# Optimization experiments

Hardware: AMD Instinct MI355X
Metric: run time of the kernel (lower is better)

Reference implementation:

```python
import jax, jax.numpy as jnp
import numpy as np

B, C, D, J = 8, 2048, 128, 128

def setup_inputs() -> dict:
    key = jax.random.key(0)
    ks = jax.random.split(key, 24)
    s = 0.02
    inp = {
        "operation_features": jax.random.normal(ks[0], (B, C, D), jnp.float32),
        "relations": jax.random.randint(ks[1], (B, C - 2, 2), 0, C, jnp.int64),
        "begins_idx": jax.random.randint(ks[2], (B, J), 0, C, jnp.int64),
        "ends_idx": jax.random.randint(ks[3], (B, J), 0, C, jnp.int64),
        "same_type_mask": (jax.random.uniform(ks[4], (B, C, C)) > 0.5).astype(jnp.float32),
        # BeginEndEncoder
        "W_begin": jax.random.normal(ks[5], (D, D), jnp.float32) * s,
        "b_begin": jnp.zeros((D,), jnp.float32),
        "W_end": jax.random.normal(ks[6], (D, D), jnp.float32) * s,
        "b_end": jnp.zeros((D,), jnp.float32),
        # OperationTimeRelationEncoder.mix: Linear(3D -> D)
        "W_mix3": jax.random.normal(ks[7], (3 * D, D), jnp.float32) * s,
        "b_mix3": jnp.zeros((D,), jnp.float32),
        # SelfAttention (hidden_dim = D)
        "W_qkv": jax.random.normal(ks[8], (D, 3 * D), jnp.float32) * s,
        "b_qkv": jnp.zeros((3 * D,), jnp.float32),
        "w_score": jax.random.normal(ks[9], (2 * D,), jnp.float32) * s,
        "b_score": jnp.zeros((), jnp.float32),
        "W_out": jax.random.normal(ks[10], (D, D), jnp.float32) * s,
        "b_out": jnp.zeros((D,), jnp.float32),
        # block mix: Linear(2D -> D)
        "W_mix2": jax.random.normal(ks[11], (2 * D, D), jnp.float32) * s,
        "b_mix2": jnp.zeros((D,), jnp.float32),
    }
    return inp

def _gather_ops(ops, idx):
    # ops: [B,C,D], idx: [B,M] -> [B,M,D]  (torch.gather along dim 1 with expanded index)
    Bb, _, Dd = ops.shape
    M = idx.shape[1]
    return jnp.take_along_axis(ops, jnp.broadcast_to(idx[:, :, None], (Bb, M, Dd)), axis=1)

def reference(operation_features, relations, begins_idx, ends_idx, same_type_mask,
              W_begin, b_begin, W_end, b_end, W_mix3, b_mix3,
              W_qkv, b_qkv, w_score, b_score, W_out, b_out, W_mix2, b_mix2):
    ops = operation_features
    Dd = ops.shape[-1]
    # --- OperationTimeRelationEncoder ---
    pred = _gather_ops(ops, relations[..., 0])      # [B,C-2,D]
    succ = _gather_ops(ops, relations[..., 1])      # [B,C-2,D]
    concated = jnp.concatenate([ops[:, :-2, :], pred, succ], axis=-1)  # [B,C-2,3D]
    mixed = concated @ W_mix3 + b_mix3              # [B,C-2,D]
    begin_f = _gather_ops(ops, begins_idx) @ W_begin + b_begin  # [B,J,D]
    end_f = _gather_ops(ops, ends_idx) @ W_end + b_end
    begin = jnp.mean(begin_f, axis=1)               # [B,D]
    end = jnp.mean(end_f, axis=1)
    seq = jnp.concatenate([mixed, begin[:, None, :], end[:, None, :]], axis=1)  # [B,C,D]
    # --- SelfAttention (GAT-style additive score, decomposed to avoid CxCx2h blowup) ---
    qkv = ops @ W_qkv + b_qkv                       # [B,C,3D]
    q, k, v = jnp.split(qkv, 3, axis=-1)
    sq = q @ w_score[:Dd]                           # [B,C]  q_i . w_q
    sk = k @ w_score[Dd:]                           # [B,C]  k_j . w_k
    scores = jax.nn.leaky_relu(sq[:, :, None] + sk[:, None, :] + b_score)  # [B,C,C]
    attn = jax.nn.softmax(scores * same_type_mask, axis=-1)                # multiplicative mask, as in torch
    weighted = jnp.einsum('bij,bjd->bid', attn, v)  # [B,C,D]
    same_type = weighted @ W_out + b_out            # [B,C,D]
    # --- final mix ---
    return jnp.concatenate([seq, same_type], axis=-1) @ W_mix2 + b_mix2  # [B,C,D]
```

## Files before the change

### kernel.cpp

```cpp
#include <hip/hip_runtime.h>
#include <cstddef>

typedef __bf16 bf16;
typedef __bf16 bf16x4 __attribute__((ext_vector_type(4)));
typedef __bf16 bf16x8 __attribute__((ext_vector_type(8)));
typedef float  f32x4  __attribute__((ext_vector_type(4)));

#define MFMA16(a, b, c) __builtin_amdgcn_mfma_f32_16x16x32_bf16((a), (b), (c), 0, 0, 0)

#define BB 8
#define CC 2048
#define DD 128
#define JJN 128

#define WS_PK    ((size_t)0)
#define WS_OATT  ((size_t)4194304)
#define WS_OPS16 ((size_t)8388608)
#define WS_SQF   ((size_t)12582912)
#define WS_SKF   ((size_t)12648448)
#define WS_G1T   ((size_t)12713984)
#define WS_G2T   ((size_t)12746752)
#define WS_G3T   ((size_t)12779520)
#define WS_WCT   ((size_t)12812288)
#define WS_GBT   ((size_t)12845056)
#define WS_GET   ((size_t)12877824)
#define WS_UQK   ((size_t)12910592)
#define WS_BBM   ((size_t)12911104)
#define WS_BBB   ((size_t)12911616)
#define WS_BBE   ((size_t)12912128)
#define WS_SC    ((size_t)12912640)
#define WS_WCN   ((size_t)12913152)
#define WS_GBN   ((size_t)12945920)
#define WS_GEN   ((size_t)12978688)

__global__ __launch_bounds__(256) void k_prepcast(
    const float* __restrict__ ops, bf16* __restrict__ ops16,
    const float* __restrict__ Wmix3, const float* __restrict__ Wmix2,
    const float* __restrict__ Wout,  const float* __restrict__ Wbegin,
    const float* __restrict__ Wend,  const float* __restrict__ Wqkv,
    const float* __restrict__ bqkv,  const float* __restrict__ wscore,
    const float* __restrict__ bscore,const float* __restrict__ bmix3,
    const float* __restrict__ bout,  const float* __restrict__ bmix2,
    const float* __restrict__ bbegin,const float* __restrict__ bend,
    bf16* __restrict__ G1T, bf16* __restrict__ G2T, bf16* __restrict__ G3T,
    bf16* __restrict__ WCT, bf16* __restrict__ GBT, bf16* __restrict__ GET,
    bf16* __restrict__ WCN, bf16* __restrict__ GBN, bf16* __restrict__ GEN,
    bf16* __restrict__ uqk, float* __restrict__ BBM, float* __restrict__ BBB,
    float* __restrict__ BBE, float* __restrict__ sc)
{
    __shared__ bf16  LshT[128 * 132];
    __shared__ float Rsh[128 * 8];
    int wg = blockIdx.x;
    int t  = threadIdx.x;

    if (wg == 0) {
        for (int half = 0; half < 2; ++half) {
            #pragma unroll
            for (int pass = 0; pass < 16; ++pass) {
                int idx = pass * 256 + t;
                int d   = idx >> 5;
                int e0  = (idx & 31) * 4;
                f32x4 v = *(const f32x4*)(Wqkv + d*384 + half*128 + e0);
                #pragma unroll
                for (int jj = 0; jj < 4; ++jj)
                    LshT[(e0 + jj)*132 + d] = (bf16)v[jj];
            }
            if (t < 32) {
                f32x4 wv = *(const f32x4*)(wscore + half*128 + t*4);
                #pragma unroll
                for (int jj = 0; jj < 4; ++jj) Rsh[t*4 + jj] = wv[jj];
            }
            __syncthreads();
            if (t < 128) {
                float s = 0.f;
                for (int e = 0; e < 128; ++e)
                    s += (float)LshT[e*132 + t] * Rsh[e];
                uqk[half*128 + t] = (bf16)s;
            }
            __syncthreads();
        }
        float bm = 0.f, bb_ = 0.f, be_ = 0.f, bon = 0.f;
        for (int half = 0; half < 2; ++half) {
            #pragma unroll
            for (int pass = 0; pass < 16; ++pass) {
                int idx = pass * 256 + t;
                int f   = idx >> 5;
                int e0  = (idx & 31) * 4;
                f32x4 v = *(const f32x4*)(Wmix2 + (size_t)(half*128 + f)*128 + e0);
                #pragma unroll
                for (int jj = 0; jj < 4; ++jj)
                    LshT[f*132 + e0 + jj] = (bf16)v[jj];
            }
            if (t < 32) {
                if (half == 0) {
                    f32x4 v0 = *(const f32x4*)(bmix3  + t*4);
                    f32x4 v1 = *(const f32x4*)(bbegin + t*4);
                    f32x4 v2 = *(const f32x4*)(bend   + t*4);
                    #pragma unroll
                    for (int jj = 0; jj < 4; ++jj) {
                        Rsh[t*4 + jj]       = v0[jj];
                        Rsh[128 + t*4 + jj] = v1[jj];
                        Rsh[256 + t*4 + jj] = v2[jj];
                    }
                } else {
                    f32x4 v3 = *(const f32x4*)(bout + t*4);
                    #pragma unroll
                    for (int jj = 0; jj < 4; ++jj) Rsh[t*4 + jj] = v3[jj];
                }
            }
            __syncthreads();
            if (t < 128) {
                if (half == 0) {
                    for (int f = 0; f < 128; ++f) {
                        float wv = (float)LshT[f*132 + t];
                        bm  += Rsh[f]       * wv;
                        bb_ += Rsh[128 + f] * wv;
                        be_ += Rsh[256 + f] * wv;
                    }
                } else {
                    for (int f = 0; f < 128; ++f)
                        bon += Rsh[f] * (float)LshT[f*132 + t];
                }
            }
            __syncthreads();
        }
        if (t < 128) {
            float bm2 = bmix2[t];
            BBM[t] = bm  + bon + bm2;
            BBB[t] = bb_ + bon + bm2;
            BBE[t] = be_ + bon + bm2;
        }
        if (t >= 128) {
            int e2 = t - 128;
            Rsh[512 + e2] = bqkv[e2]       * wscore[e2];
            Rsh[640 + e2] = bqkv[128 + e2] * wscore[128 + e2];
        }
        __syncthreads();
        if (t == 0) {
            float cq = 0.f, ck = 0.f;
            for (int e2 = 0; e2 < 128; ++e2) {
                cq += Rsh[512 + e2];
                ck += Rsh[640 + e2];
            }
            sc[0] = cq + bscore[0];
            sc[1] = ck;
        }
        return;
    }
    if (wg <= 96) {
        int id  = wg - 1;
        int mat = id >> 4, sub = id & 15;
        const float* L; const float* R; bf16* O; bf16* O2;
        switch (mat) {
            case 0: L = Wmix3;           R = Wmix2;           O = G1T; O2 = nullptr; break;
            case 1: L = Wmix3 + 128*128; R = Wmix2;           O = G2T; O2 = nullptr; break;
            case 2: L = Wmix3 + 256*128; R = Wmix2;           O = G3T; O2 = nullptr; break;
            case 3: L = Wout;            R = Wmix2 + 128*128; O = WCT; O2 = WCN; break;
            case 4: L = Wbegin;          R = Wmix2;           O = GBT; O2 = GBN; break;
            default:L = Wend;            R = Wmix2;           O = GET; O2 = GEN; break;
        }
        int e0 = sub * 8;
        #pragma unroll
        for (int pass = 0; pass < 16; ++pass) {
            int idx = pass * 256 + t;
            int d   = idx >> 5;
            int f0  = (idx & 31) * 4;
            f32x4 v = *(const f32x4*)(L + d * 128 + f0);
            #pragma unroll
            for (int jj = 0; jj < 4; ++jj)
                LshT[(f0 + jj) * 132 + d] = (bf16)v[jj];
        }
        #pragma unroll
        for (int pass = 0; pass < 4; ++pass) {
            int idx = pass * 256 + t;
            int f   = idx >> 3;
            int ee  = idx & 7;
            Rsh[f * 8 + ee] = R[f * 128 + e0 + ee];
        }
        __syncthreads();
        int ee = t >> 5;
        int e  = e0 + ee;
        int d0 = (t & 31) * 4;
        float s[4] = {0.f, 0.f, 0.f, 0.f};
        for (int f = 0; f < 128; ++f) {
            bf16x4 lv = *(const bf16x4*)&LshT[f * 132 + d0];
            float rv = Rsh[f * 8 + ee];
            #pragma unroll
            for (int dd = 0; dd < 4; ++dd)
                s[dd] += (float)lv[dd] * rv;
        }
        #pragma unroll
        for (int dd = 0; dd < 4; ++dd) {
            O[e * 128 + d0 + dd] = (bf16)s[dd];
            if (O2) O2[(d0 + dd) * 128 + e] = (bf16)s[dd];
        }
        return;
    }
    size_t i = (size_t)(wg - 97) * 256 + t;
    f32x4 a = *(const f32x4*)(ops + i * 8);
    f32x4 b = *(const f32x4*)(ops + i * 8 + 4);
    bf16x8 o;
    #pragma unroll
    for (int e = 0; e < 4; ++e) { o[e] = (bf16)a[e]; o[4 + e] = (bf16)b[e]; }
    *(bf16x8*)(ops16 + i * 8) = o;
}

__global__ __launch_bounds__(256) void k_v(
    const bf16* __restrict__ ops16, const float* __restrict__ Wqkv,
    const float* __restrict__ bqkv, const bf16* __restrict__ uqk,
    const float* __restrict__ sc,
    bf16* __restrict__ PK, float* __restrict__ sqf, float* __restrict__ skf)
{
    __shared__ bf16 A[144 * 136];
    int b  = blockIdx.x >> 4;
    int jt = (blockIdx.x & 15) * 128;
    int t  = threadIdx.x;
    #pragma unroll
    for (int pass = 0; pass < 16; ++pass) {
        int idx = pass * 256 + t;
        int d   = idx >> 5;
        int n0  = (idx & 31) * 4;
        f32x4 v = *(const f32x4*)(Wqkv + d*384 + 256 + n0);
        #pragma unroll
        for (int jj = 0; jj < 4; ++jj)
            A[(n0 + jj)*136 + d] = (bf16)v[jj];
    }
    {
        int row = t >> 7, col = t & 127;
        A[(128 + row)*136 + col] = uqk[row*128 + col];
    }
    for (int idx = t; idx < 14*136; idx += 256)
        A[130*136 + idx] = (bf16)0.f;
    __syncthreads();

    int lane = t & 63, w = t >> 6;
    int m = lane & 15, q = lane >> 4;
    f32x4 acc[9][2];
    #pragma unroll
    for (int rb = 0; rb < 9; ++rb)
        #pragma unroll
        for (int cb = 0; cb < 2; ++cb)
            acc[rb][cb] = {0.f, 0.f, 0.f, 0.f};

    const bf16* opsb = ops16 + (size_t)b * CC * DD;
    #pragma unroll
    for (int kc = 0; kc < 4; ++kc) {
        bf16x8 bfr[2];
        #pragma unroll
        for (int cb = 0; cb < 2; ++cb) {
            int j = jt + w*32 + cb*16 + m;
            bfr[cb] = *(const bf16x8*)(opsb + (size_t)j*DD + kc*32 + q*8);
        }
        #pragma unroll
        for (int rb = 0; rb < 9; ++rb) {
            bf16x8 afr = *(const bf16x8*)&A[(rb*16 + m)*136 + kc*32 + q*8];
            acc[rb][0] = MFMA16(afr, bfr[0], acc[rb][0]);
            acc[rb][1] = MFMA16(afr, bfr[1], acc[rb][1]);
        }
    }
    float cqb = sc[0], ckv = sc[1];
    #pragma unroll
    for (int cb = 0; cb < 2; ++cb) {
        int j = jt + w*32 + cb*16 + m;
        if (q == 0) {
            sqf[b*CC + j] = acc[8][cb][0] + cqb;
            skf[b*CC + j] = acc[8][cb][1] + ckv;
        }
    }
    __syncthreads();
    bf16* pack = A;
    #pragma unroll
    for (int cb = 0; cb < 2; ++cb) {
        int qq_base = cb*2 + (m>>3);
        int e       = m & 7;
        #pragma unroll
        for (int rb = 0; rb < 8; ++rb) {
            #pragma unroll
            for (int r = 0; r < 4; ++r) {
                float v = acc[rb][cb][r] + bqkv[256 + rb*16 + q*4 + r];
                pack[w*4096 + rb*512 + qq_base*128 + (q*4+r)*8 + e] = (bf16)v;
            }
        }
    }
    __syncthreads();
    bf16* pkb = PK + (size_t)b * DD * CC + (size_t)jt * 128;
    #pragma unroll
    for (int pass = 0; pass < 8; ++pass) {
        int lidx = pass * 256 + t;
        *(uint4*)(pkb + (size_t)lidx * 8) = *(const uint4*)&pack[lidx * 8];
    }
}

struct MaskLd { f32x4 v[8]; };

__device__ __forceinline__ MaskLd stage_load(const float* __restrict__ mrow0,
                                             int st, int lane)
{
    MaskLd L;
    int rr0 = lane >> 4, cc = (lane & 15) * 4;
    const float* src = mrow0 + st * 64 + cc;
    #pragma unroll
    for (int k = 0; k < 8; ++k)
        L.v[k] = __builtin_nontemporal_load(
            (const f32x4*)(src + ((size_t)(rr0 + k * 4)) * CC));
    return L;
}

__device__ __forceinline__ void stage_write(const MaskLd& L, bf16* mb,
                                            int buf, int lane)
{
    int rr0 = lane >> 4, cc = (lane & 15) * 4;
    bf16* dst = mb + buf * 2816;
    #pragma unroll
    for (int k = 0; k < 8; ++k) {
        bf16x4 o;
        #pragma unroll
        for (int e = 0; e < 4; ++e) o[e] = (bf16)L.v[k][e];
        *(bf16x4*)(dst + (rr0 + k * 4) * 88 + cc) = o;
    }
}

__device__ __forceinline__ void load_vb(const bf16* __restrict__ pkb, int jc,
                                        int q, int m, bf16x8 vb[8])
{
    #pragma unroll
    for (int nb = 0; nb < 8; ++nb)
        vb[nb] = *(const bf16x8*)(pkb + ((size_t)(((jc*8 + nb)*4 + q)*16 + m)) * 8);
}

__device__ __forceinline__ void substep(const bf16* mb, const float* skb,
    int buf, int st, int sub, int tile, int q, int m, float sq,
    const bf16x8 vb[8], float& lsum, f32x4 acc[8])
{
    bf16x8 mk = *(const bf16x8*)(mb + buf * 2816 + (tile*16 + m) * 88
                                 + sub * 32 + q * 8);
    int jo = st * 64 + sub * 32 + q * 8;
    f32x4 s0 = *(const f32x4*)(skb + jo);
    f32x4 s1 = *(const f32x4*)(skb + jo + 4);
    float sks[8] = {s0[0], s0[1], s0[2], s0[3], s1[0], s1[1], s1[2], s1[3]};
    bf16x8 a;
    #pragma unroll
    for (int e = 0; e < 8; ++e) {
        float tv = sq + sks[e];
        float lr = fmaxf(tv, 0.01f * tv);
        float z  = lr * (float)mk[e];
        float p  = __expf(z);
        lsum += p;
        a[e] = (bf16)p;
    }
    #pragma unroll
    for (int nb = 0; nb < 8; ++nb)
        acc[nb] = MFMA16(a, vb[nb], acc[nb]);
}

__global__ __launch_bounds__(256) void k_att(
    const float* __restrict__ mask, const bf16* __restrict__ PK,
    const float* __restrict__ sqf, const float* __restrict__ skf,
    bf16* __restrict__ Oatt)
{
    __shared__ __align__(16) char smem[53248];
    int t    = threadIdx.x;
    int lane = t & 63, w = t >> 6;
    int b    = blockIdx.x & 7;
    int i0   = (blockIdx.x >> 3) << 5;
    int m = lane & 15, q = lane >> 4;

    bf16*  mbuf = (bf16*)(smem + w * 11264);
    float* skb  = (float*)(smem + 45056 + w * 2048);

    {
        const float* src = skf + b*CC + w*512;
        f32x4 v0 = *(const f32x4*)(src + lane*4);
        f32x4 v1 = *(const f32x4*)(src + 256 + lane*4);
        *(f32x4*)(skb + lane*4) = v0;
        *(f32x4*)(skb + 256 + lane*4) = v1;
    }
    float sq0 = sqf[b*CC + i0 + m];
    float sq1 = sqf[b*CC + i0 + 16 + m];
    const float* mrow0 = mask + ((size_t)(b*CC + i0))*CC + w*512;
    const bf16*  pkb   = PK + (size_t)b * DD * CC;
    int jc0 = w * 16;

    f32x4 acc0[8], acc1[8];
    #pragma unroll
    for (int nb = 0; nb < 8; ++nb) {
        acc0[nb] = {0.f, 0.f, 0.f, 0.f};
        acc1[nb] = {0.f, 0.f, 0.f, 0.f};
    }
    float lsum0 = 0.f, lsum1 = 0.f;

    {   MaskLd r0 = stage_load(mrow0, 0, lane);
        stage_write(r0, mbuf, 0, lane); }
    MaskLd r1 = stage_load(mrow0, 1, lane);
    MaskLd r2 = stage_load(mrow0, 2, lane);

    int buf = 0;
    for (int st = 0; st < 8; ++st) {
        #pragma unroll
        for (int sub = 0; sub < 2; ++sub) {
            bf16x8 vb[8];
            load_vb(pkb, jc0 + st*2 + sub, q, m, vb);
            substep(mbuf, skb, buf, st, sub, 0, q, m, sq0, vb, lsum0, acc0);
            substep(mbuf, skb, buf, st, sub, 1, q, m, sq1, vb, lsum1, acc1);
        }
        if (st + 1 < 8) stage_write(r1, mbuf, buf ^ 1, lane);
        r1 = r2;
        if (st + 3 < 8) r2 = stage_load(mrow0, st + 3, lane);
        buf ^= 1;
    }

    __syncthreads();
    float* Osh = (float*)smem;
    float* Lsh = (float*)(smem + 33792);
    #pragma unroll
    for (int tile = 0; tile < 2; ++tile) {
        float ls = tile ? lsum1 : lsum0;
        ls += __shfl_xor(ls, 16, 64);
        ls += __shfl_xor(ls, 32, 64);
        if (q == 0) Lsh[w*16 + m] = ls;
        const f32x4* acc = tile ? acc1 : acc0;
        #pragma unroll
        for (int nb = 0; nb < 8; ++nb)
            #pragma unroll
            for (int r = 0; r < 4; ++r)
                Osh[(w*16 + q*4 + r)*132 + nb*16 + m] = acc[nb][r];
        __syncthreads();

        int r  = t >> 4;
        int c0 = (t & 15) * 8;
        float l = Lsh[r] + Lsh[16 + r] + Lsh[32 + r] + Lsh[48 + r];
        float inv = 1.0f / l;
        bf16x8 o;
        #pragma unroll
        for (int e = 0; e < 8; ++e) {
            float s = Osh[r*132 + c0 + e] + Osh[(16 + r)*132 + c0 + e]
                    + Osh[(32 + r)*132 + c0 + e] + Osh[(48 + r)*132 + c0 + e];
            o[e] = (bf16)(s * inv);
        }
        *(bf16x8*)(Oatt + ((size_t)(b*CC) + i0 + tile*16 + r)*DD + c0) = o;
        if (tile == 0) __syncthreads();
    }
}

__global__ __launch_bounds__(256) void k_epi(
    const bf16* __restrict__ ops16, const int* __restrict__ relations,
    const int* __restrict__ begins, const int* __restrict__ ends,
    const bf16* __restrict__ Oatt,
    const bf16* __restrict__ G1T, const bf16* __restrict__ G2T,
    const bf16* __restrict__ G3T, const bf16* __restrict__ WCT,
    const bf16* __restrict__ GBN, const bf16* __restrict__ GEN,
    const bf16* __restrict__ WCN,
    const float* __restrict__ BBM, const float* __restrict__ BBB,
    const float* __restrict__ BBE, float* __restrict__ out)
{
    __shared__ bf16 Abuf[32 * 136];
    __shared__ bf16 Bbuf[128 * 136];
    int t  = threadIdx.x;

    if (blockIdx.x < 8) {
        __shared__ float meanv[2][128];
        int eidx  = blockIdx.x * 2 + (t >> 7);
        int b     = eidx >> 1, which = eidx & 1;
        int tl    = t & 127;
        const int* idx = which ? (ends + b*JJN) : (begins + b*JJN);
        const bf16* opsb = ops16 + (size_t)b * CC * DD;
        float s0 = 0.f, s1 = 0.f;
        for (int j = 0; j < JJN; j += 2) {
            int r0 = idx[j], r1 = idx[j+1];
            s0 += (float)opsb[(size_t)r0*DD + tl];
            s1 += (float)opsb[(size_t)r1*DD + tl];
        }
        meanv[t >> 7][tl] = (s0 + s1) * (1.0f / (float)JJN);
        __syncthreads();
        const bf16* G   = which ? GEN : GBN;
        const float* Bv = which ? BBE : BBB;
        const bf16* orow = Oatt + ((size_t)b*CC + (CC - 2 + which)) * DD;
        float a = Bv[tl];
        const float* mv = meanv[t >> 7];
        for (int d = 0; d < 128; ++d) {
            a += mv[d] * (float)G[d*128 + tl];
            a += (float)orow[d] * (float)WCN[d*128 + tl];
        }
        out[((size_t)b*CC + (CC - 2 + which))*DD + tl] = a;
        return;
    }

    int gid = blockIdx.x - 8;
    int b  = gid >> 6;
    int c0 = (gid & 63) * 32;
    int lane = t & 63, w = t >> 6;
    int m = lane & 15, q = lane >> 4;

    f32x4 acc[2][2];
    #pragma unroll
    for (int rb = 0; rb < 2; ++rb)
        #pragma unroll
        for (int cb = 0; cb < 2; ++cb)
            acc[rb][cb] = {0.f, 0.f, 0.f, 0.f};

    const bf16* Bsrc[4] = {G1T, G2T, G3T, WCT};
    int arow = t >> 3, ao = (t & 7) * 16;
    int brow = t >> 1, bo = (t & 1) * 64;
    int c = c0 + arow;

    for (int term = 0; term < 4; ++term) {
        const bf16* src;
        if (term == 0)      src = ops16 + ((size_t)(b*CC + c)) * DD;
        else if (term == 3) src = Oatt  + ((size_t)(b*CC + c)) * DD;
        else {
            int ridx = relations[((size_t)b*(CC-2) + min(c, CC-3))*2 + (term - 1)];
            src = ops16 + ((size_t)(b*CC) + ridx) * DD;
        }
        *(uint4*)&Abuf[arow*136 + ao]     = *(const uint4*)(src + ao);
        *(uint4*)&Abuf[arow*136 + ao + 8] = *(const uint4*)(src + ao + 8);

        const uint4* bs = (const uint4*)(Bsrc[term] + brow*128 + bo);
        uint4* bd = (uint4*)&Bbuf[brow*136 + bo];
        #pragma unroll
        for (int ii = 0; ii < 8; ++ii) bd[ii] = bs[ii];
        __syncthreads();

        #pragma unroll
        for (int kc = 0; kc < 4; ++kc) {
            bf16x8 bfr[2];
            #pragma unroll
            for (int cb = 0; cb < 2; ++cb)
                bfr[cb] = *(const bf16x8*)&Bbuf[(w*32 + cb*16 + m)*136 + kc*32 + q*8];
            #pragma unroll
            for (int rb = 0; rb < 2; ++rb) {
                bf16x8 afr = *(const bf16x8*)&Abuf[(rb*16 + m)*136 + kc*32 + q*8];
                acc[rb][0] = MFMA16(afr, bfr[0], acc[rb][0]);
                acc[rb][1] = MFMA16(afr, bfr[1], acc[rb][1]);
            }
        }
        __syncthreads();
    }
    #pragma unroll
    for (int cb = 0; cb < 2; ++cb) {
        int col = w*32 + cb*16 + m;
        float bias = BBM[col];
        #pragma unroll
        for (int rb = 0; rb < 2; ++rb) {
            #pragma unroll
            for (int r = 0; r < 4; ++r) {
                int cg = c0 + rb*16 + q*4 + r;
                if (cg < CC - 2)
                    out[((size_t)(b*CC) + cg)*DD + col] = acc[rb][cb][r] + bias;
            }
        }
    }
}

extern "C" void kernel_launch(void* const* d_in, const int* in_sizes, int n_in,
                              void* d_out, int out_size, void* d_ws, size_t ws_size,
                              hipStream_t stream)
{
    const float* ops      = (const float*)d_in[0];
    const int*  relations = (const int*)d_in[1];
    const int*  begins    = (const int*)d_in[2];
    const int*  ends      = (const int*)d_in[3];
    const float* mask     = (const float*)d_in[4];
    const float* Wbegin   = (const float*)d_in[5];
    const float* bbegin   = (const float*)d_in[6];
    const float* Wend     = (const float*)d_in[7];
    const float* bend     = (const float*)d_in[8];
    const float* Wmix3    = (const float*)d_in[9];
    const float* bmix3    = (const float*)d_in[10];
    const float* Wqkv     = (const float*)d_in[11];
    const float* bqkv     = (const float*)d_in[12];
    const float* wscore   = (const float*)d_in[13];
    const float* bscore   = (const float*)d_in[14];
    const float* Wout     = (const float*)d_in[15];
    const float* bout     = (const float*)d_in[16];
    const float* Wmix2    = (const float*)d_in[17];
    const float* bmix2    = (const float*)d_in[18];
    float* outp = (float*)d_out;

    char* ws = (char*)d_ws;
    bf16*  PK    = (bf16*)(ws + WS_PK);
    bf16*  Oatt  = (bf16*)(ws + WS_OATT);
    bf16*  OPS16 = (bf16*)(ws + WS_OPS16);
    float* sqf   = (float*)(ws + WS_SQF);
    float* skf   = (float*)(ws + WS_SKF);
    bf16*  G1T   = (bf16*)(ws + WS_G1T);
    bf16*  G2T   = (bf16*)(ws + WS_G2T);
    bf16*  G3T   = (bf16*)(ws + WS_G3T);
    bf16*  WCT   = (bf16*)(ws + WS_WCT);
    bf16*  GBT   = (bf16*)(ws + WS_GBT);
    bf16*  GET   = (bf16*)(ws + WS_GET);
    bf16*  WCN   = (bf16*)(ws + WS_WCN);
    bf16*  GBN   = (bf16*)(ws + WS_GBN);
    bf16*  GEN   = (bf16*)(ws + WS_GEN);
    bf16*  UQK   = (bf16*)(ws + WS_UQK);
    float* BBM   = (float*)(ws + WS_BBM);
    float* BBB   = (float*)(ws + WS_BBB);
    float* BBE   = (float*)(ws + WS_BBE);
    float* SC    = (float*)(ws + WS_SC);

    k_prepcast<<<dim3(1121), dim3(256), 0, stream>>>(
        ops, OPS16,
        Wmix3, Wmix2, Wout, Wbegin, Wend, Wqkv, bqkv, wscore, bscore,
        bmix3, bout, bmix2, bbegin, bend,
        G1T, G2T, G3T, WCT, GBT, GET, WCN, GBN, GEN,
        UQK, BBM, BBB, BBE, SC);

    k_v<<<dim3(128), dim3(256), 0, stream>>>(
        OPS16, Wqkv, bqkv, UQK, SC, PK, sqf, skf);

    k_att<<<dim3(512), dim3(256), 0, stream>>>(
        mask, PK, sqf, skf, Oatt);

    k_epi<<<dim3(520), dim3(256), 0, stream>>>(
        OPS16, relations, begins, ends, Oatt,
        G1T, G2T, G3T, WCT, GBN, GEN, WCN, BBM, BBB, BBE, outp);
}
```

Baseline: 283.4 us.

## Pre-pack mask to bits and fuse attention with epilogue GEMM

The float mask is converted to a packed bitmask in the prep kernel, and the attention loop reads mask bytes from LDS instead of staging float tiles. The attention and epilogue kernels are merged so the normalized attention output stays in shared memory rather than round-tripping through global memory. The begin/end means are also moved into the prep kernel. Binarizing assumes the mask holds only zeros and ones, and the full mask read now happens before attention instead of overlapping with it.

Result: faster. 275.2 us (median of 2 runs) (-2.9%).

```diff
diff --git a/kernel.cpp b/kernel.cpp
--- a/kernel.cpp
+++ b/kernel.cpp
@@ -32,9 +32,13 @@
 #define WS_WCN   ((size_t)12913152)
 #define WS_GBN   ((size_t)12945920)
 #define WS_GEN   ((size_t)12978688)
+#define WS_MB    ((size_t)13011456)
+#define WS_MEANV ((size_t)17205760)
 
 __global__ __launch_bounds__(256) void k_prepcast(
     const float* __restrict__ ops, bf16* __restrict__ ops16,
+    const float* __restrict__ mask, const int* __restrict__ begins,
+    const int* __restrict__ ends,
     const float* __restrict__ Wmix3, const float* __restrict__ Wmix2,
     const float* __restrict__ Wout,  const float* __restrict__ Wbegin,
     const float* __restrict__ Wend,  const float* __restrict__ Wqkv,
@@ -46,7 +50,8 @@
     bf16* __restrict__ WCT, bf16* __restrict__ GBT, bf16* __restrict__ GET,
     bf16* __restrict__ WCN, bf16* __restrict__ GBN, bf16* __restrict__ GEN,
     bf16* __restrict__ uqk, float* __restrict__ BBM, float* __restrict__ BBB,
-    float* __restrict__ BBE, float* __restrict__ sc)
+    float* __restrict__ BBE, float* __restrict__ sc,
+    unsigned char* __restrict__ MBITS, float* __restrict__ MEANV)
 {
     __shared__ bf16  LshT[128 * 132];
     __shared__ float Rsh[128 * 8];
@@ -147,8 +152,50 @@
         }
         return;
     }
-    if (wg <= 96) {
-        int id  = wg - 1;
+    if (wg <= 16) {
+        int task = wg - 1;
+        int b2 = task >> 1, which = task & 1;
+        const int* idxp = which ? (ends + b2 * JJN) : (begins + b2 * JJN);
+        int* ish = (int*)Rsh;
+        if (t < JJN) ish[t] = idxp[t];
+        __syncthreads();
+        int d = t & 127, half = t >> 7;
+        const float* opsb = ops + (size_t)b2 * CC * DD;
+        float s = 0.f;
+        #pragma unroll 8
+        for (int j = 0; j < 64; ++j) {
+            int r = ish[half * 64 + j];
+            s += opsb[(size_t)r * DD + d];
+        }
+        float* fsh = Rsh + 256;
+        fsh[half * 128 + d] = s;
+        __syncthreads();
+        if (t < 128)
+            MEANV[task * 128 + t] = (fsh[t] + fsh[128 + t]) * (1.0f / (float)JJN);
+        return;
+    }
+    if (wg <= 2064) {
+        int p = wg - 17;
+        size_t base = (size_t)p * 16384;
+        const float* mp = mask + base;
+        unsigned char* ob = MBITS + (base >> 3);
+        #pragma unroll
+        for (int k = 0; k < 8; ++k) {
+            size_t fo = (size_t)k * 2048 + (size_t)t * 8;
+            f32x4 a = __builtin_nontemporal_load((const f32x4*)(mp + fo));
+            f32x4 c = __builtin_nontemporal_load((const f32x4*)(mp + fo + 4));
+            unsigned byte = 0;
+            #pragma unroll
+            for (int e = 0; e < 4; ++e) {
+                byte |= (a[e] != 0.f ? 1u : 0u) << e;
+                byte |= (c[e] != 0.f ? 1u : 0u) << (4 + e);
+            }
+            ob[k * 256 + t] = (unsigned char)byte;
+        }
+        return;
+    }
+    if (wg <= 2160) {
+        int id  = wg - 2065;
         int mat = id >> 4, sub = id & 15;
         const float* L; const float* R; bf16* O; bf16* O2;
         switch (mat) {
@@ -196,7 +243,7 @@
         }
         return;
     }
-    size_t i = (size_t)(wg - 97) * 256 + t;
+    size_t i = (size_t)(wg - 2161) * 256 + t;
     f32x4 a = *(const f32x4*)(ops + i * 8);
     f32x4 b = *(const f32x4*)(ops + i * 8 + 4);
     bf16x8 o;
@@ -291,35 +338,6 @@
     }
 }
 
-struct MaskLd { f32x4 v[8]; };
-
-__device__ __forceinline__ MaskLd stage_load(const float* __restrict__ mrow0,
-                                             int st, int lane)
-{
-    MaskLd L;
-    int rr0 = lane >> 4, cc = (lane & 15) * 4;
-    const float* src = mrow0 + st * 64 + cc;
-    #pragma unroll
-    for (int k = 0; k < 8; ++k)
-        L.v[k] = __builtin_nontemporal_load(
-            (const f32x4*)(src + ((size_t)(rr0 + k * 4)) * CC));
-    return L;
-}
-
-__device__ __forceinline__ void stage_write(const MaskLd& L, bf16* mb,
-                                            int buf, int lane)
-{
-    int rr0 = lane >> 4, cc = (lane & 15) * 4;
-    bf16* dst = mb + buf * 2816;
-    #pragma unroll
-    for (int k = 0; k < 8; ++k) {
-        bf16x4 o;
-        #pragma unroll
-        for (int e = 0; e < 4; ++e) o[e] = (bf16)L.v[k][e];
-        *(bf16x4*)(dst + (rr0 + k * 4) * 88 + cc) = o;
-    }
-}
-
 __device__ __forceinline__ void load_vb(const bf16* __restrict__ pkb, int jc,
                                         int q, int m, bf16x8 vb[8])
 {
@@ -328,12 +346,10 @@
         vb[nb] = *(const bf16x8*)(pkb + ((size_t)(((jc*8 + nb)*4 + q)*16 + m)) * 8);
 }
 
-__device__ __forceinline__ void substep(const bf16* mb, const float* skb,
-    int buf, int st, int sub, int tile, int q, int m, float sq,
+__device__ __forceinline__ void substep(const float* __restrict__ skb,
+    unsigned mbyte, int st, int sub, int q, float sq,
     const bf16x8 vb[8], float& lsum, f32x4 acc[8])
 {
-    bf16x8 mk = *(const bf16x8*)(mb + buf * 2816 + (tile*16 + m) * 88
-                                 + sub * 32 + q * 8);
     int jo = st * 64 + sub * 32 + q * 8;
     f32x4 s0 = *(const f32x4*)(skb + jo);
     f32x4 s1 = *(const f32x4*)(skb + jo + 4);
@@ -343,8 +359,8 @@
     for (int e = 0; e < 8; ++e) {
         float tv = sq + sks[e];
         float lr = fmaxf(tv, 0.01f * tv);
-        float z  = lr * (float)mk[e];
-        float p  = __expf(z);
+        float pm = (float)((mbyte >> e) & 1u);
+        float p  = __expf(lr * pm);
         lsum += p;
         a[e] = (bf16)p;
     }
@@ -353,32 +369,46 @@
         acc[nb] = MFMA16(a, vb[nb], acc[nb]);
 }
 
-__global__ __launch_bounds__(256) void k_att(
-    const float* __restrict__ mask, const bf16* __restrict__ PK,
+__global__ __launch_bounds__(256) void k_attepi(
+    const unsigned char* __restrict__ MBITS, const bf16* __restrict__ PK,
     const float* __restrict__ sqf, const float* __restrict__ skf,
-    bf16* __restrict__ Oatt)
+    const bf16* __restrict__ ops16, const int* __restrict__ relations,
+    const bf16* __restrict__ G1T, const bf16* __restrict__ G2T,
+    const bf16* __restrict__ G3T, const bf16* __restrict__ WCT,
+    const bf16* __restrict__ GBN, const bf16* __restrict__ GEN,
+    const bf16* __restrict__ WCN,
+    const float* __restrict__ BBM, const float* __restrict__ BBB,
+    const float* __restrict__ BBE, const float* __restrict__ MEANV,
+    float* __restrict__ out)
 {
-    __shared__ __align__(16) char smem[53248];
+    __shared__ __align__(16) char smem[52224];
     int t    = threadIdx.x;
     int lane = t & 63, w = t >> 6;
     int b    = blockIdx.x & 7;
     int i0   = (blockIdx.x >> 3) << 5;
     int m = lane & 15, q = lane >> 4;
 
-    bf16*  mbuf = (bf16*)(smem + w * 11264);
-    float* skb  = (float*)(smem + 45056 + w * 2048);
+    unsigned char* Lb  = (unsigned char*)smem;
+    float*         skb = (float*)(smem + 8704 + w * 2048);
 
     {
-        const float* src = skf + b*CC + w*512;
-        f32x4 v0 = *(const f32x4*)(src + lane*4);
-        f32x4 v1 = *(const f32x4*)(src + 256 + lane*4);
-        *(f32x4*)(skb + lane*4) = v0;
-        *(f32x4*)(skb + 256 + lane*4) = v1;
-    }
-    float sq0 = sqf[b*CC + i0 + m];
-    float sq1 = sqf[b*CC + i0 + 16 + m];
-    const float* mrow0 = mask + ((size_t)(b*CC + i0))*CC + w*512;
-    const bf16*  pkb   = PK + (size_t)b * DD * CC;
+        int row = t >> 3, seg = t & 7;
+        const uint4* src = (const uint4*)(MBITS
+            + ((size_t)(b * CC + i0 + row)) * 256 + seg * 32);
+        uint4 v0 = src[0], v1 = src[1];
+        *(uint4*)(Lb + row * 272 + seg * 32)      = v0;
+        *(uint4*)(Lb + row * 272 + seg * 32 + 16) = v1;
+    }
+    {
+        const float* src = skf + b * CC + w * 512;
+        f32x4 v0 = *(const f32x4*)(src + lane * 4);
+        f32x4 v1 = *(const f32x4*)(src + 256 + lane * 4);
+        *(f32x4*)(skb + lane * 4)       = v0;
+        *(f32x4*)(skb + 256 + lane * 4) = v1;
+    }
+    float sq0 = sqf[b * CC + i0 + m];
+    float sq1 = sqf[b * CC + i0 + 16 + m];
+    const bf16* pkb = PK + (size_t)b * DD * CC;
     int jc0 = w * 16;
 
     f32x4 acc0[8], acc1[8];
@@ -388,166 +418,134 @@
         acc1[nb] = {0.f, 0.f, 0.f, 0.f};
     }
     float lsum0 = 0.f, lsum1 = 0.f;
-
-    {   MaskLd r0 = stage_load(mrow0, 0, lane);
-        stage_write(r0, mbuf, 0, lane); }
-    MaskLd r1 = stage_load(mrow0, 1, lane);
-    MaskLd r2 = stage_load(mrow0, 2, lane);
-
-    int buf = 0;
+    __syncthreads();
+
     for (int st = 0; st < 8; ++st) {
         #pragma unroll
         for (int sub = 0; sub < 2; ++sub) {
             bf16x8 vb[8];
-            load_vb(pkb, jc0 + st*2 + sub, q, m, vb);
-            substep(mbuf, skb, buf, st, sub, 0, q, m, sq0, vb, lsum0, acc0);
-            substep(mbuf, skb, buf, st, sub, 1, q, m, sq1, vb, lsum1, acc1);
-        }
-        if (st + 1 < 8) stage_write(r1, mbuf, buf ^ 1, lane);
-        r1 = r2;
-        if (st + 3 < 8) r2 = stage_load(mrow0, st + 3, lane);
-        buf ^= 1;
+            load_vb(pkb, jc0 + st * 2 + sub, q, m, vb);
+            int bo = w * 64 + st * 8 + sub * 4 + q;
+            unsigned mb0 = Lb[m * 272 + bo];
+            unsigned mb1 = Lb[(16 + m) * 272 + bo];
+            substep(skb, mb0, st, sub, q, sq0, vb, lsum0, acc0);
+            substep(skb, mb1, st, sub, q, sq1, vb, lsum1, acc1);
+        }
     }
 
     __syncthreads();
-    float* Osh = (float*)smem;
-    float* Lsh = (float*)(smem + 33792);
+    float* Osh  = (float*)(smem + 8704);
+    float* Lsh  = (float*)(smem + 42496);
+    bf16*  Obuf = (bf16*)(smem + 43520);
     #pragma unroll
     for (int tile = 0; tile < 2; ++tile) {
         float ls = tile ? lsum1 : lsum0;
         ls += __shfl_xor(ls, 16, 64);
         ls += __shfl_xor(ls, 32, 64);
-        if (q == 0) Lsh[w*16 + m] = ls;
+        if (q == 0) Lsh[w * 16 + m] = ls;
         const f32x4* acc = tile ? acc1 : acc0;
         #pragma unroll
         for (int nb = 0; nb < 8; ++nb)
             #pragma unroll
             for (int r = 0; r < 4; ++r)
-                Osh[(w*16 + q*4 + r)*132 + nb*16 + m] = acc[nb][r];
-        __syncthreads();
-
-        int r  = t >> 4;
-        int c0 = (t & 15) * 8;
+                Osh[(w * 16 + q * 4 + r) * 132 + nb * 16 + m] = acc[nb][r];
+        __syncthreads();
+
+        int r   = t >> 4;
+        int c0e = (t & 15) * 8;
         float l = Lsh[r] + Lsh[16 + r] + Lsh[32 + r] + Lsh[48 + r];
         float inv = 1.0f / l;
         bf16x8 o;
         #pragma unroll
         for (int e = 0; e < 8; ++e) {
-            float s = Osh[r*132 + c0 + e] + Osh[(16 + r)*132 + c0 + e]
-                    + Osh[(32 + r)*132 + c0 + e] + Osh[(48 + r)*132 + c0 + e];
+            float s = Osh[r * 132 + c0e + e] + Osh[(16 + r) * 132 + c0e + e]
+                    + Osh[(32 + r) * 132 + c0e + e] + Osh[(48 + r) * 132 + c0e + e];
             o[e] = (bf16)(s * inv);
         }
-        *(bf16x8*)(Oatt + ((size_t)(b*CC) + i0 + tile*16 + r)*DD + c0) = o;
-        if (tile == 0) __syncthreads();
-    }
-}
-
-__global__ __launch_bounds__(256) void k_epi(
-    const bf16* __restrict__ ops16, const int* __restrict__ relations,
-    const int* __restrict__ begins, const int* __restrict__ ends,
-    const bf16* __restrict__ Oatt,
-    const bf16* __restrict__ G1T, const bf16* __restrict__ G2T,
-    const bf16* __restrict__ G3T, const bf16* __restrict__ WCT,
-    const bf16* __restrict__ GBN, const bf16* __restrict__ GEN,
-    const bf16* __restrict__ WCN,
-    const float* __restrict__ BBM, const float* __restrict__ BBB,
-    const float* __restrict__ BBE, float* __restrict__ out)
-{
-    __shared__ bf16 Abuf[32 * 136];
-    __shared__ bf16 Bbuf[128 * 136];
-    int t  = threadIdx.x;
-
-    if (blockIdx.x < 8) {
-        __shared__ float meanv[2][128];
-        int eidx  = blockIdx.x * 2 + (t >> 7);
-        int b     = eidx >> 1, which = eidx & 1;
-        int tl    = t & 127;
-        const int* idx = which ? (ends + b*JJN) : (begins + b*JJN);
-        const bf16* opsb = ops16 + (size_t)b * CC * DD;
-        float s0 = 0.f, s1 = 0.f;
-        for (int j = 0; j < JJN; j += 2) {
-            int r0 = idx[j], r1 = idx[j+1];
-            s0 += (float)opsb[(size_t)r0*DD + tl];
-            s1 += (float)opsb[(size_t)r1*DD + tl];
-        }
-        meanv[t >> 7][tl] = (s0 + s1) * (1.0f / (float)JJN);
-        __syncthreads();
-        const bf16* G   = which ? GEN : GBN;
-        const float* Bv = which ? BBE : BBB;
-        const bf16* orow = Oatt + ((size_t)b*CC + (CC - 2 + which)) * DD;
-        float a = Bv[tl];
-        const float* mv = meanv[t >> 7];
-        for (int d = 0; d < 128; ++d) {
-            a += mv[d] * (float)G[d*128 + tl];
-            a += (float)orow[d] * (float)WCN[d*128 + tl];
-        }
-        out[((size_t)b*CC + (CC - 2 + which))*DD + tl] = a;
-        return;
-    }
-
-    int gid = blockIdx.x - 8;
-    int b  = gid >> 6;
-    int c0 = (gid & 63) * 32;
-    int lane = t & 63, w = t >> 6;
-    int m = lane & 15, q = lane >> 4;
-
-    f32x4 acc[2][2];
+        *(bf16x8*)&Obuf[(tile * 16 + r) * 136 + c0e] = o;
+        __syncthreads();
+    }
+
+    bf16* Abuf = (bf16*)smem;
+    bf16* Bbuf = (bf16*)(smem + 8704);
+
+    f32x4 eacc[2][2];
     #pragma unroll
     for (int rb = 0; rb < 2; ++rb)
         #pragma unroll
         for (int cb = 0; cb < 2; ++cb)
-            acc[rb][cb] = {0.f, 0.f, 0.f, 0.f};
+            eacc[rb][cb] = {0.f, 0.f, 0.f, 0.f};
 
     const bf16* Bsrc[4] = {G1T, G2T, G3T, WCT};
     int arow = t >> 3, ao = (t & 7) * 16;
-    int brow = t >> 1, bo = (t & 1) * 64;
-    int c = c0 + arow;
+    int brow = t >> 1, bo2 = (t & 1) * 64;
+    int c = i0 + arow;
 
     for (int term = 0; term < 4; ++term) {
-        const bf16* src;
-        if (term == 0)      src = ops16 + ((size_t)(b*CC + c)) * DD;
-        else if (term == 3) src = Oatt  + ((size_t)(b*CC + c)) * DD;
-        else {
-            int ridx = relations[((size_t)b*(CC-2) + min(c, CC-3))*2 + (term - 1)];
-            src = ops16 + ((size_t)(b*CC) + ridx) * DD;
-        }
-        *(uint4*)&Abuf[arow*136 + ao]     = *(const uint4*)(src + ao);
-        *(uint4*)&Abuf[arow*136 + ao + 8] = *(const uint4*)(src + ao + 8);
-
-        const uint4* bs = (const uint4*)(Bsrc[term] + brow*128 + bo);
-        uint4* bd = (uint4*)&Bbuf[brow*136 + bo];
+        if (term < 3) {
+            const bf16* src;
+            if (term == 0) src = ops16 + ((size_t)(b * CC + c)) * DD;
+            else {
+                int ridx = relations[((size_t)b * (CC - 2) + min(c, CC - 3)) * 2 + (term - 1)];
+                src = ops16 + ((size_t)(b * CC) + ridx) * DD;
+            }
+            *(uint4*)&Abuf[arow * 136 + ao]     = *(const uint4*)(src + ao);
+            *(uint4*)&Abuf[arow * 136 + ao + 8] = *(const uint4*)(src + ao + 8);
+        }
+        const uint4* bs = (const uint4*)(Bsrc[term] + brow * 128 + bo2);
+        uint4* bd = (uint4*)&Bbuf[brow * 136 + bo2];
         #pragma unroll
         for (int ii = 0; ii < 8; ++ii) bd[ii] = bs[ii];
         __syncthreads();
 
+        const bf16* Asrc = (term == 3) ? Obuf : Abuf;
         #pragma unroll
         for (int kc = 0; kc < 4; ++kc) {
             bf16x8 bfr[2];
             #pragma unroll
             for (int cb = 0; cb < 2; ++cb)
-                bfr[cb] = *(const bf16x8*)&Bbuf[(w*32 + cb*16 + m)*136 + kc*32 + q*8];
+                bfr[cb] = *(const bf16x8*)&Bbuf[(w * 32 + cb * 16 + m) * 136 + kc * 32 + q * 8];
             #pragma unroll
             for (int rb = 0; rb < 2; ++rb) {
-                bf16x8 afr = *(const bf16x8*)&Abuf[(rb*16 + m)*136 + kc*32 + q*8];
-                acc[rb][0] = MFMA16(afr, bfr[0], acc[rb][0]);
-                acc[rb][1] = MFMA16(afr, bfr[1], acc[rb][1]);
+                bf16x8 afr = *(const bf16x8*)&Asrc[(rb * 16 + m) * 136 + kc * 32 + q * 8];
+                eacc[rb][0] = MFMA16(afr, bfr[0], eacc[rb][0]);
+                eacc[rb][1] = MFMA16(afr, bfr[1], eacc[rb][1]);
             }
         }
         __syncthreads();
     }
     #pragma unroll
     for (int cb = 0; cb < 2; ++cb) {
-        int col = w*32 + cb*16 + m;
+        int col = w * 32 + cb * 16 + m;
         float bias = BBM[col];
         #pragma unroll
         for (int rb = 0; rb < 2; ++rb) {
             #pragma unroll
             for (int r = 0; r < 4; ++r) {
-                int cg = c0 + rb*16 + q*4 + r;
+                int cg = i0 + rb * 16 + q * 4 + r;
                 if (cg < CC - 2)
-                    out[((size_t)(b*CC) + cg)*DD + col] = acc[rb][cb][r] + bias;
-            }
-        }
+                    out[((size_t)(b * CC) + cg) * DD + col] = eacc[rb][cb][r] + bias;
+            }
+        }
+    }
+
+    if (i0 == CC - 32) {
+        __syncthreads();
+        float* mv2 = (float*)smem;
+        int grp = t >> 7, tl = t & 127;
+        mv2[grp * 128 + tl] = MEANV[((size_t)b * 2 + grp) * 128 + tl];
+        __syncthreads();
+        int which = grp;
+        const bf16* G    = which ? GEN : GBN;
+        const float* Bv  = which ? BBE : BBB;
+        const bf16* orow = Obuf + (30 + which) * 136;
+        float a = Bv[tl];
+        const float* mv = mv2 + grp * 128;
+        for (int d = 0; d < 128; ++d) {
+            a += mv[d] * (float)G[d * 128 + tl];
+            a += (float)orow[d] * (float)WCN[d * 128 + tl];
+        }
+        out[((size_t)b * CC + (CC - 2 + which)) * DD + tl] = a;
     }
 }
 
@@ -578,7 +576,6 @@
 
     char* ws = (char*)d_ws;
     bf16*  PK    = (bf16*)(ws + WS_PK);
-    bf16*  Oatt  = (bf16*)(ws + WS_OATT);
     bf16*  OPS16 = (bf16*)(ws + WS_OPS16);
     float* sqf   = (float*)(ws + WS_SQF);
     float* skf   = (float*)(ws + WS_SKF);
@@ -596,21 +593,20 @@
     float* BBB   = (float*)(ws + WS_BBB);
     float* BBE   = (float*)(ws + WS_BBE);
     float* SC    = (float*)(ws + WS_SC);
-
-    k_prepcast<<<dim3(1121), dim3(256), 0, stream>>>(
-        ops, OPS16,
+    unsigned char* MBITS = (unsigned char*)(ws + WS_MB);
+    float* MEANV = (float*)(ws + WS_MEANV);
+
+    k_prepcast<<<dim3(3185), dim3(256), 0, stream>>>(
+        ops, OPS16, mask, begins, ends,
         Wmix3, Wmix2, Wout, Wbegin, Wend, Wqkv, bqkv, wscore, bscore,
         bmix3, bout, bmix2, bbegin, bend,
         G1T, G2T, G3T, WCT, GBT, GET, WCN, GBN, GEN,
-        UQK, BBM, BBB, BBE, SC);
+        UQK, BBM, BBB, BBE, SC, MBITS, MEANV);
 
     k_v<<<dim3(128), dim3(256), 0, stream>>>(
         OPS16, Wqkv, bqkv, UQK, SC, PK, sqf, skf);
 
-    k_att<<<dim3(512), dim3(256), 0, stream>>>(
-        mask, PK, sqf, skf, Oatt);
-
-    k_epi<<<dim3(520), dim3(256), 0, stream>>>(
-        OPS16, relations, begins, ends, Oatt,
-        G1T, G2T, G3T, WCT, GBN, GEN, WCN, BBM, BBB, BBE, outp);
+    k_attepi<<<dim3(512), dim3(256), 0, stream>>>(
+        MBITS, PK, sqf, skf, OPS16, relations,
+        G1T, G2T, G3T, WCT, GBN, GEN, WCN, BBM, BBB, BBE, MEANV, outp);
 }
```
